# Kernel optimization log

Hardware: AMD Instinct MI355X
Metric: run time of the kernel (lower is better)

## Reference

```python
import math
import jax, jax.numpy as jnp
import numpy as np

# ---- SLAYER neuron / simulation constants (from config) ----
THETA = 10.0      # spike threshold
TAU_SR = 10.0     # PSP (SRM) kernel time constant
TAU_REF = 1.0     # refractory kernel time constant
TS = 1.0          # simulation time step
T_SAMPLE = 500    # number of time bins
B, N_IN, N_HID, N_OUT = 64, 1024, 1024, 10


def _alpha_kernel(tau, mult, eps=0.01):
    """slayer _calculateAlphaKernel: mult * t/tau * exp(1 - t/tau), truncated."""
    vals = []
    t = 0.0
    while t < T_SAMPLE:
        v = mult * t / tau * math.exp(1.0 - t / tau)
        if abs(v) < eps and t > tau:
            break
        vals.append(v)
        t += TS
    return np.asarray(vals, np.float32)

SRM_KERNEL = jnp.asarray(_alpha_kernel(TAU_SR, 1.0))            # [K]
REF_KERNEL = jnp.asarray(_alpha_kernel(TAU_REF, -2.0 * THETA))  # [Kr], REF_KERNEL[0] == 0


def dense(x, W):
    # per-timestep fully-connected layer (slayer.dense == 1x1x1 conv3d, no bias)
    # x: [B, Nin, T], W: [Nout, Nin] -> [B, Nout, T]
    return jnp.einsum('oi,bit->bot', W, x)


def psp(x):
    # causal temporal convolution with the SRM kernel: out[t] = Ts * sum_k srm[k] * x[t-k]
    Bx, N, T = x.shape
    K = SRM_KERNEL.shape[0]
    k = SRM_KERNEL[::-1].reshape(1, 1, K).astype(x.dtype)  # flip -> true convolution
    y = jax.lax.conv_general_dilated(
        x.reshape(Bx * N, 1, T), k, (1,), [(K - 1, 0)],
        dimension_numbers=('NCH', 'OIH', 'NCH'))
    return y.reshape(Bx, N, T) * TS


def spike_impl(u_in):
    # sequential LIF thresholding with refractory feedback (slayer spike kernel)
    # u_in: [B, N, T] membrane drive; returns (spikes, membrane) both [B, N, T]
    Kr = REF_KERNEL.shape[0]
    # buf[j] is the refractory contribution arriving at step t+j; new spike at t
    # contributes REF_KERNEL[j] at t+j (REF_KERNEL[0]==0), i.e. shifted kernel into buf.
    refk = jnp.concatenate([REF_KERNEL[1:], jnp.zeros((1,), u_in.dtype)]).astype(u_in.dtype)
    buf0 = jnp.zeros(u_in.shape[:-1] + (Kr,), u_in.dtype)

    def step(buf, u_t):
        u = u_t + buf[..., 0]                              # membrane at time t
        s = (u >= THETA).astype(u_in.dtype) / TS           # spike (amplitude 1/Ts)
        buf = jnp.concatenate([buf[..., 1:], jnp.zeros_like(buf[..., :1])], axis=-1)
        buf = buf + s[..., None] * refk
        return buf, (s, u)

    _, (s, u) = jax.lax.scan(step, buf0, jnp.moveaxis(u_in, -1, 0))
    return jnp.moveaxis(s, 0, -1), jnp.moveaxis(u, 0, -1)


def setup_inputs() -> dict:
    key = jax.random.key(0)
    k1, k2, k3 = jax.random.split(key, 3)
    spike_input = (jax.random.uniform(k1, (B, N_IN, T_SAMPLE)) < 0.05).astype(jnp.float32)
    W1 = jax.random.normal(k2, (N_HID, N_IN), jnp.float32) * 0.3
    W2 = jax.random.normal(k3, (N_OUT, N_HID), jnp.float32) * 0.3
    return {"spike_input": spike_input, "W1": W1, "W2": W2}


def reference(spike_input, W1, W2):
    s1, _ = spike_impl(psp(dense(spike_input, W1)))
    s2, _ = spike_impl(psp(dense(s1, W2)))
    return s2
```

## Files before the change

### kernel.cpp

```cpp
#include <hip/hip_runtime.h>
#include <stdint.h>
#include <math.h>

#define T_SIM 500
#define NB    64
#define NIN   1024
#define NHID  1024
#define NOUT  10
#define KSRM  77
#define CHUNK 32
#define TT5   12
#define NT5   42
#define RING5 128

__device__ __forceinline__ double srm_tap(int k) {
  double u = (double)k / 10.0;
  double v = u * exp(1.0 - u);
  return (double)(float)v;
}
__device__ __forceinline__ double ref_tap(int j) {
  double v = (-20.0 * (double)j) * exp(1.0 - (double)j);
  return (double)(float)v;
}

__global__ __launch_bounds__(64)
void k_pack(const float* __restrict__ x, unsigned long long* __restrict__ bits) {
  const int b = blockIdx.x, ig = blockIdx.y, tc = blockIdx.z;
  const int lane = threadIdx.x;
  const float* xr = x + ((size_t)b * NIN + ig * 64 + lane) * T_SIM;
  const int t0 = tc * 100;
  for (int t = t0; t < t0 + 100; t += 4) {
    const float4 v = *(const float4*)(xr + t);
    unsigned long long m0 = __ballot(v.x > 0.5f);
    unsigned long long m1 = __ballot(v.y > 0.5f);
    unsigned long long m2 = __ballot(v.z > 0.5f);
    unsigned long long m3 = __ballot(v.w > 0.5f);
    if (lane == 0) {
      unsigned long long* w = bits + (size_t)(b * T_SIM + t) * 16 + ig;
      w[0] = m0; w[16] = m1; w[32] = m2; w[48] = m3;
    }
  }
}

__global__ __launch_bounds__(256)
void k_transpose(const float* __restrict__ W1, float* __restrict__ W1T) {
  __shared__ float tile[64][65];
  const int bo = blockIdx.x * 64, bi = blockIdx.y * 64;
  for (int k = threadIdx.x; k < 4096; k += 256) {
    int r = k >> 6, c = k & 63;
    tile[r][c] = W1[(size_t)(bo + r) * NIN + bi + c];
  }
  __syncthreads();
  for (int k = threadIdx.x; k < 4096; k += 256) {
    int r = k >> 6, c = k & 63;
    W1T[(size_t)(bi + r) * NHID + bo + c] = tile[c][r];
  }
}

__global__ __launch_bounds__(128)
void k_dense1(const uint32_t* __restrict__ bits, const float* __restrict__ W1T,
              double* __restrict__ a1c, int col_base) {
  __shared__ int list[NIN];
  __shared__ int nact_s;
  const int col_loc = blockIdx.x;
  const int tid = threadIdx.x;
  if (tid < 32) {
    uint32_t w = bits[(size_t)(col_base + col_loc) * 32 + tid];
    int c = __popc(w);
    int p = c;
#pragma unroll
    for (int d = 1; d < 32; d <<= 1) {
      int q = __shfl_up(p, d);
      if (tid >= d) p += q;
    }
    int excl = p - c;
    while (w) {
      const int j = __ffs(w) - 1;
      w &= w - 1;
      list[excl++] = tid * 32 + j;
    }
    if (tid == 31) nact_s = excl;
  }
  __syncthreads();
  const int n = nact_s;
  const int o = blockIdx.y * 512 + tid * 4;
  double ax[4] = {0,0,0,0}, ay[4] = {0,0,0,0};
  double az[4] = {0,0,0,0}, aw[4] = {0,0,0,0};
  float4 L[8];
  int g = 0;
  if (n >= 8) {
#pragma unroll
    for (int r = 0; r < 8; ++r)
      L[r] = *(const float4*)(W1T + (size_t)list[r] * NHID + o);
    for (g = 0; g + 16 <= n; g += 8) {
      float4 Nb[8];
#pragma unroll
      for (int r = 0; r < 8; ++r)
        Nb[r] = *(const float4*)(W1T + (size_t)list[g + 8 + r] * NHID + o);
#pragma unroll
      for (int r = 0; r < 8; ++r) {
        const int s = r & 3;
        ax[s] += (double)L[r].x; ay[s] += (double)L[r].y;
        az[s] += (double)L[r].z; aw[s] += (double)L[r].w;
      }
#pragma unroll
      for (int r = 0; r < 8; ++r) L[r] = Nb[r];
    }
#pragma unroll
    for (int r = 0; r < 8; ++r) {
      const int s = r & 3;
      ax[s] += (double)L[r].x; ay[s] += (double)L[r].y;
      az[s] += (double)L[r].z; aw[s] += (double)L[r].w;
    }
    g += 8;
  }
  for (; g < n; ++g) {
    const float4 wv = *(const float4*)(W1T + (size_t)list[g] * NHID + o);
    const int s = g & 3;
    ax[s] += (double)wv.x; ay[s] += (double)wv.y;
    az[s] += (double)wv.z; aw[s] += (double)wv.w;
  }
  double* dst = a1c + (size_t)col_loc * NHID + o;
  __builtin_nontemporal_store((ax[0] + ax[1]) + (ax[2] + ax[3]), dst + 0);
  __builtin_nontemporal_store((ay[0] + ay[1]) + (ay[2] + ay[3]), dst + 1);
  __builtin_nontemporal_store((az[0] + az[1]) + (az[2] + az[3]), dst + 2);
  __builtin_nontemporal_store((aw[0] + aw[1]) + (aw[2] + aw[3]), dst + 3);
}

__global__ __launch_bounds__(448)
void k_ps1(const double* __restrict__ a1c, uint32_t* __restrict__ s1w,
           int b_base) {
  __shared__ double S[RING5 * 32];
  __shared__ double Yp[2][4][TT5 * 32];
  __shared__ double TB[80];
  const int ng = blockIdx.x, b_loc = blockIdx.y;
  const int tid = threadIdx.x;
  const double* __restrict__ abase = a1c + (size_t)b_loc * T_SIM * NHID + ng * 32;
  uint32_t* __restrict__ sbase = s1w + (size_t)(b_base + b_loc) * T_SIM * 32 + ng;

  if (tid < 80) TB[tid] = (tid <= 76) ? srm_tap(tid) : 0.0;
  for (int i = tid; i < RING5 * 32; i += 448) S[i] = 0.0;
  __syncthreads();
  for (int id = tid; id < TT5 * 32; id += 448) {
    const int r = id >> 5, nn = id & 31;
    S[r * 32 + nn] = abase[(size_t)r * NHID + nn];
  }

  const bool isFIR = (tid < 384);
  const int g   = tid / 96;
  const int rem = tid - g * 96;
  const int q   = rem >> 5;
  const int n   = rem & 31;
  double tap[20];
  __syncthreads();
  if (isFIR) {
#pragma unroll
    for (int j = 0; j < 20; ++j) tap[j] = TB[20 * g + j];
  }
  double refk[11];
#pragma unroll
  for (int j = 1; j <= 10; ++j) refk[j] = ref_tap(j);
  uint32_t smask = 0;

  for (int k = 0; k < NT5; ++k) {
    const int t0 = k * TT5;
    const int tv = (T_SIM - t0 < TT5) ? (T_SIM - t0) : TT5;
    const int t0n = t0 + TT5;
    const int tvn = (t0n >= T_SIM) ? 0 : ((T_SIM - t0n < TT5) ? (T_SIM - t0n) : TT5);
    if (isFIR) {
      double pf = 0.0;
      const int pr = tid >> 5, pn = tid & 31;
      const bool hasPf = (tid < tvn * 32);
      if (hasPf) pf = abase[(size_t)(t0n + pr) * NHID + pn];
      const int tb = t0 + q * 4;
      int slot = (tb - 20 * g - 19 + 1024) & (RING5 - 1);
      double a0 = 0, a1 = 0, a2 = 0, a3 = 0;
#pragma unroll
      for (int s = 0; s < 23; ++s) {
        const double v = S[slot * 32 + n];
        slot = (slot + 1) & (RING5 - 1);
        if (s <= 19)           a0 += tap[19 - s] * v;
        if (s >= 1 && s <= 20) a1 += tap[20 - s] * v;
        if (s >= 2 && s <= 21) a2 += tap[21 - s] * v;
        if (s >= 3)            a3 += tap[22 - s] * v;
      }
      double* Yk = Yp[k & 1][g];
      const int tl = q * 4;
      if (tl + 0 < tv) Yk[(tl + 0) * 32 + n] = a0;
      if (tl + 1 < tv) Yk[(tl + 1) * 32 + n] = a1;
      if (tl + 2 < tv) Yk[(tl + 2) * 32 + n] = a2;
      if (tl + 3 < tv) Yk[(tl + 3) * 32 + n] = a3;
      if (hasPf) S[((t0n + pr) & (RING5 - 1)) * 32 + pn] = pf;
    } else if (k > 0) {
      const int lane = tid - 384;
      if (lane < 32) {
        const int t0p = t0 - TT5;
        const double* Y0 = Yp[(k - 1) & 1][0];
        const double* Y1 = Yp[(k - 1) & 1][1];
        const double* Y2 = Yp[(k - 1) & 1][2];
        const double* Y3 = Yp[(k - 1) & 1][3];
        for (int gg = 0; gg < TT5; ++gg) {
          double u = (Y0[gg * 32 + lane] + Y1[gg * 32 + lane]) +
                     (Y2[gg * 32 + lane] + Y3[gg * 32 + lane]);
#pragma unroll
          for (int j = 10; j >= 1; --j)
            u += refk[j] * (double)((smask >> (j - 1)) & 1u);
          const bool sp = (u >= 10.0);
          smask = (smask << 1) | (sp ? 1u : 0u);
          const unsigned long long bm = __ballot(sp);
          if (lane == 0) sbase[(size_t)(t0p + gg) * 32] = (uint32_t)bm;
        }
      }
    }
    __syncthreads();
  }
  if (!isFIR) {
    const int lane = tid - 384;
    if (lane < 32) {
      const int t0p = (NT5 - 1) * TT5;
      const int tvp = T_SIM - t0p;
      const double* Y0 = Yp[(NT5 - 1) & 1][0];
      const double* Y1 = Yp[(NT5 - 1) & 1][1];
      const double* Y2 = Yp[(NT5 - 1) & 1][2];
      const double* Y3 = Yp[(NT5 - 1) & 1][3];
      for (int gg = 0; gg < tvp; ++gg) {
        double u = (Y0[gg * 32 + lane] + Y1[gg * 32 + lane]) +
                   (Y2[gg * 32 + lane] + Y3[gg * 32 + lane]);
#pragma unroll
        for (int j = 10; j >= 1; --j)
          u += refk[j] * (double)((smask >> (j - 1)) & 1u);
        const bool sp = (u >= 10.0);
        smask = (smask << 1) | (sp ? 1u : 0u);
        const unsigned long long bm = __ballot(sp);
        if (lane == 0) sbase[(size_t)(t0p + gg) * 32] = (uint32_t)bm;
      }
    }
  }
}

__global__ __launch_bounds__(256)
void k_dense2(const uint32_t* __restrict__ s1w,
              const float* __restrict__ W2, double* __restrict__ a2) {
  __shared__ float w2t[NHID * NOUT];
  for (int k = threadIdx.x; k < NHID * NOUT; k += 256) {
    const int o = k >> 10, i = k & 1023;
    w2t[i * NOUT + o] = W2[k];
  }
  __syncthreads();
  const int col = blockIdx.x * 256 + threadIdx.x;
  double acc[NOUT];
#pragma unroll
  for (int o = 0; o < NOUT; ++o) acc[o] = 0.0;
  const uint32_t* w = s1w + (size_t)col * 32;
  for (int wi = 0; wi < 32; ++wi) {
    uint32_t m = w[wi];
    const int ibase = wi * 32;
    while (m) {
      const int j = __ffs(m) - 1;
      m &= m - 1;
      const float* row = &w2t[(ibase + j) * NOUT];
#pragma unroll
      for (int o = 0; o < NOUT; ++o) acc[o] += (double)row[o];
    }
  }
  double* outp = a2 + (size_t)col * NOUT;
#pragma unroll
  for (int o = 0; o < NOUT; ++o) outp[o] = acc[o];
}

__global__ __launch_bounds__(256)
void k_l2(const double* __restrict__ a2, float* __restrict__ out) {
  __shared__ double S[T_SIM * NOUT];
  __shared__ double Y[T_SIM * NOUT];
  __shared__ double srm[KSRM];
  const int b = blockIdx.x, tid = threadIdx.x;
  if (tid < KSRM) srm[tid] = srm_tap(tid);
  for (int i = tid; i < T_SIM * NOUT; i += 256)
    S[i] = a2[(size_t)b * T_SIM * NOUT + i];
  __syncthreads();
  for (int i = tid; i < T_SIM * NOUT; i += 256) {
    const int t = i / 10, o = i - t * 10;
    const int kmax = (t < KSRM - 1) ? t : (KSRM - 1);
    double acc = 0.0;
    for (int k = 0; k <= kmax; ++k)
      acc += srm[k] * S[(t - k) * 10 + o];
    Y[i] = acc;
  }
  __syncthreads();
  if (tid < NOUT) {
    double refk[11];
#pragma unroll
    for (int j = 1; j <= 10; ++j) refk[j] = ref_tap(j);
    uint32_t smask = 0;
    float* op = out + ((size_t)b * NOUT + tid) * T_SIM;
    for (int t = 0; t < T_SIM; ++t) {
      double u = Y[t * 10 + tid];
#pragma unroll
      for (int j = 10; j >= 1; --j)
        u += refk[j] * (double)((smask >> (j - 1)) & 1u);
      const bool sp = (u >= 10.0);
      smask = (smask << 1) | (sp ? 1u : 0u);
      op[t] = sp ? 1.0f : 0.0f;
    }
  }
}

extern "C" void kernel_launch(void* const* d_in, const int* in_sizes, int n_in,
                              void* d_out, int out_size, void* d_ws, size_t ws_size,
                              hipStream_t stream) {
  const float* x  = (const float*)d_in[0];
  const float* W1 = (const float*)d_in[1];
  const float* W2 = (const float*)d_in[2];
  float* out = (float*)d_out;

  char* ws = (char*)d_ws;
  unsigned long long* bits1 = (unsigned long long*)(ws);
  float*  W1T = (float*) (ws + 4096000);
  double* a1c = (double*)(ws + 8290304);
  uint32_t* s1w = (uint32_t*)(ws + 139362304);
  double* a2  = (double*)(ws + 143458304);

  hipLaunchKernelGGL(k_pack, dim3(NB, 16, 5), dim3(64), 0, stream, x, bits1);
  hipLaunchKernelGGL(k_transpose, dim3(16, 16), dim3(256), 0, stream, W1, W1T);

  for (int bc = 0; bc < NB; bc += CHUNK) {
    hipLaunchKernelGGL(k_dense1, dim3(CHUNK * T_SIM, 2), dim3(128), 0, stream,
                       (const uint32_t*)bits1, W1T, a1c, bc * T_SIM);
    hipLaunchKernelGGL(k_ps1, dim3(32, CHUNK), dim3(448), 0, stream,
                       a1c, s1w, bc);
  }

  hipLaunchKernelGGL(k_dense2, dim3(125), dim3(256), 0, stream, s1w, W2, a2);
  hipLaunchKernelGGL(k_l2, dim3(NB), dim3(256), 0, stream, a2, out);
}
```

Measured before the change: 951.4 us.

## Fuse sparse dense1 gather into PSP/spike kernel using precomputed active lists

Replaces the separate k_dense1 pass, which wrote a large double-precision activation buffer to global memory, and the chunked k_ps1 pass that read it back. A new k_lists kernel precomputes, per batch and timestep, the indices of active input spikes (capped at 128) plus their count. k_ps1f stages these lists in shared memory, double-buffered two tiles ahead. It gathers W1T rows on the fly into the shared PSP ring, so no intermediate activation tensor touches HBM and the batch-chunk launch loop goes away. The trade-offs are more per-block gather latency inside the sequential PSP loop, and a correctness dependence on no column having more than 128 active inputs.

```diff
diff --git a/kernel.cpp b/kernel.cpp
--- a/kernel.cpp
+++ b/kernel.cpp
@@ -8,10 +8,11 @@
 #define NHID  1024
 #define NOUT  10
 #define KSRM  77
-#define CHUNK 32
 #define TT5   12
 #define NT5   42
-#define RING5 128
+#define RINGN 128
+#define NGW   32
+#define LMAX  128
 
 __device__ __forceinline__ double srm_tap(int k) {
   double u = (double)k / 10.0;
@@ -57,15 +58,13 @@
   }
 }
 
-__global__ __launch_bounds__(128)
-void k_dense1(const uint32_t* __restrict__ bits, const float* __restrict__ W1T,
-              double* __restrict__ a1c, int col_base) {
-  __shared__ int list[NIN];
-  __shared__ int nact_s;
-  const int col_loc = blockIdx.x;
+__global__ __launch_bounds__(64)
+void k_lists(const uint32_t* __restrict__ bits, unsigned short* __restrict__ lists,
+             int* __restrict__ cnt) {
+  const int col = blockIdx.x * T_SIM + blockIdx.y;
   const int tid = threadIdx.x;
   if (tid < 32) {
-    uint32_t w = bits[(size_t)(col_base + col_loc) * 32 + tid];
+    uint32_t w = bits[(size_t)col * 32 + tid];
     int c = __popc(w);
     int p = c;
 #pragma unroll
@@ -74,93 +73,71 @@
       if (tid >= d) p += q;
     }
     int excl = p - c;
+    unsigned short* lp = lists + (size_t)col * LMAX;
     while (w) {
       const int j = __ffs(w) - 1;
       w &= w - 1;
-      list[excl++] = tid * 32 + j;
-    }
-    if (tid == 31) nact_s = excl;
-  }
-  __syncthreads();
-  const int n = nact_s;
-  const int o = blockIdx.y * 512 + tid * 4;
-  double ax[4] = {0,0,0,0}, ay[4] = {0,0,0,0};
-  double az[4] = {0,0,0,0}, aw[4] = {0,0,0,0};
-  float4 L[8];
-  int g = 0;
-  if (n >= 8) {
-#pragma unroll
-    for (int r = 0; r < 8; ++r)
-      L[r] = *(const float4*)(W1T + (size_t)list[r] * NHID + o);
-    for (g = 0; g + 16 <= n; g += 8) {
-      float4 Nb[8];
-#pragma unroll
-      for (int r = 0; r < 8; ++r)
-        Nb[r] = *(const float4*)(W1T + (size_t)list[g + 8 + r] * NHID + o);
-#pragma unroll
-      for (int r = 0; r < 8; ++r) {
-        const int s = r & 3;
-        ax[s] += (double)L[r].x; ay[s] += (double)L[r].y;
-        az[s] += (double)L[r].z; aw[s] += (double)L[r].w;
-      }
-#pragma unroll
-      for (int r = 0; r < 8; ++r) L[r] = Nb[r];
-    }
-#pragma unroll
-    for (int r = 0; r < 8; ++r) {
-      const int s = r & 3;
-      ax[s] += (double)L[r].x; ay[s] += (double)L[r].y;
-      az[s] += (double)L[r].z; aw[s] += (double)L[r].w;
-    }
-    g += 8;
-  }
-  for (; g < n; ++g) {
-    const float4 wv = *(const float4*)(W1T + (size_t)list[g] * NHID + o);
-    const int s = g & 3;
-    ax[s] += (double)wv.x; ay[s] += (double)wv.y;
-    az[s] += (double)wv.z; aw[s] += (double)wv.w;
-  }
-  double* dst = a1c + (size_t)col_loc * NHID + o;
-  __builtin_nontemporal_store((ax[0] + ax[1]) + (ax[2] + ax[3]), dst + 0);
-  __builtin_nontemporal_store((ay[0] + ay[1]) + (ay[2] + ay[3]), dst + 1);
-  __builtin_nontemporal_store((az[0] + az[1]) + (az[2] + az[3]), dst + 2);
-  __builtin_nontemporal_store((aw[0] + aw[1]) + (aw[2] + aw[3]), dst + 3);
-}
-
-__global__ __launch_bounds__(448)
-void k_ps1(const double* __restrict__ a1c, uint32_t* __restrict__ s1w,
-           int b_base) {
-  __shared__ double S[RING5 * 32];
-  __shared__ double Yp[2][4][TT5 * 32];
+      lp[excl++] = (unsigned short)(tid * 32 + j);
+    }
+    if (tid == 31) cnt[col] = excl;
+  }
+}
+
+__global__ __launch_bounds__(448, 4)
+void k_ps1f(const float* __restrict__ W1T,
+            const unsigned short* __restrict__ lists,
+            const int* __restrict__ cnt_g,
+            uint32_t* __restrict__ s1w) {
+  __shared__ double S[RINGN * NGW];
+  __shared__ double Yp[2][4][TT5 * NGW];
   __shared__ double TB[80];
-  const int ng = blockIdx.x, b_loc = blockIdx.y;
+  __shared__ unsigned short Lst[2][TT5][LMAX];
+  __shared__ int Cnt[2][TT5];
+  const int ng = blockIdx.x, b = blockIdx.y;
   const int tid = threadIdx.x;
-  const double* __restrict__ abase = a1c + (size_t)b_loc * T_SIM * NHID + ng * 32;
-  uint32_t* __restrict__ sbase = s1w + (size_t)(b_base + b_loc) * T_SIM * 32 + ng;
+  const size_t bcol0 = (size_t)b * T_SIM;
+  uint32_t* __restrict__ sbase = s1w + (size_t)b * T_SIM * 32 + ng;
+  const float* __restrict__ wb0 = W1T + ng * NGW;
 
   if (tid < 80) TB[tid] = (tid <= 76) ? srm_tap(tid) : 0.0;
-  for (int i = tid; i < RING5 * 32; i += 448) S[i] = 0.0;
-  __syncthreads();
-  for (int id = tid; id < TT5 * 32; id += 448) {
-    const int r = id >> 5, nn = id & 31;
-    S[r * 32 + nn] = abase[(size_t)r * NHID + nn];
-  }
+  for (int i = tid; i < RINGN * NGW; i += 448) S[i] = 0.0;
+  if (tid < 24) Cnt[tid / 12][tid % 12] = cnt_g[bcol0 + tid];
+  {
+    const uint32_t* lg = (const uint32_t*)lists + bcol0 * (LMAX / 2);
+    uint32_t* ll = (uint32_t*)&Lst[0][0][0];
+    for (int i = tid; i < 24 * (LMAX / 2); i += 448) ll[i] = lg[i];
+  }
+  __syncthreads();
 
   const bool isFIR = (tid < 384);
   const int g   = tid / 96;
   const int rem = tid - g * 96;
   const int q   = rem >> 5;
   const int n   = rem & 31;
+  const int tt  = tid >> 5;
+  const int nn  = tid & 31;
   double tap[20];
-  __syncthreads();
   if (isFIR) {
 #pragma unroll
     for (int j = 0; j < 20; ++j) tap[j] = TB[20 * g + j];
+    const int c = Cnt[0][tt];
+    const uint32_t* lp32 = (const uint32_t*)&Lst[0][tt][0];
+    const float* wbase = wb0 + nn;
+    double a0 = 0.0, a1 = 0.0;
+    const int c2 = c >> 1;
+    for (int j = 0; j < c2; ++j) {
+      const uint32_t pr = lp32[j];
+      a0 += (double)wbase[(size_t)(pr & 0xffffu) << 10];
+      a1 += (double)wbase[(size_t)(pr >> 16) << 10];
+    }
+    if (c & 1) a0 += (double)wbase[(size_t)Lst[0][tt][c - 1] << 10];
+    S[tt * NGW + nn] = a0 + a1;
   }
   double refk[11];
 #pragma unroll
   for (int j = 1; j <= 10; ++j) refk[j] = ref_tap(j);
   uint32_t smask = 0;
+  __syncthreads();
 
   for (int k = 0; k < NT5; ++k) {
     const int t0 = k * TT5;
@@ -168,17 +145,37 @@
     const int t0n = t0 + TT5;
     const int tvn = (t0n >= T_SIM) ? 0 : ((T_SIM - t0n < TT5) ? (T_SIM - t0n) : TT5);
     if (isFIR) {
-      double pf = 0.0;
-      const int pr = tid >> 5, pn = tid & 31;
-      const bool hasPf = (tid < tvn * 32);
-      if (hasPf) pf = abase[(size_t)(t0n + pr) * NHID + pn];
+      if (tt < tvn) {
+        const int bufn = (k + 1) & 1;
+        const int c = Cnt[bufn][tt];
+        const uint32_t* lp32 = (const uint32_t*)&Lst[bufn][tt][0];
+        const float* wbase = wb0 + nn;
+        double a0 = 0.0, a1 = 0.0;
+        const int c2 = c >> 1;
+        for (int j = 0; j < c2; ++j) {
+          const uint32_t pr = lp32[j];
+          a0 += (double)wbase[(size_t)(pr & 0xffffu) << 10];
+          a1 += (double)wbase[(size_t)(pr >> 16) << 10];
+        }
+        if (c & 1) a0 += (double)wbase[(size_t)Lst[bufn][tt][c - 1] << 10];
+        S[((t0n + tt) & (RINGN - 1)) * NGW + nn] = a0 + a1;
+      }
+      const int k2 = k + 2;
+      if (k2 < NT5) {
+        const int t2 = k2 * TT5;
+        const int tv2 = (T_SIM - t2 < TT5) ? (T_SIM - t2) : TT5;
+        if (tid < tv2) Cnt[k & 1][tid] = cnt_g[bcol0 + t2 + tid];
+        const uint32_t* lg = (const uint32_t*)lists + (bcol0 + t2) * (LMAX / 2);
+        uint32_t* ll = (uint32_t*)&Lst[k & 1][0][0];
+        for (int i = tid; i < tv2 * (LMAX / 2); i += 384) ll[i] = lg[i];
+      }
       const int tb = t0 + q * 4;
-      int slot = (tb - 20 * g - 19 + 1024) & (RING5 - 1);
+      int slot = (tb - 20 * g - 19 + 1024) & (RINGN - 1);
       double a0 = 0, a1 = 0, a2 = 0, a3 = 0;
 #pragma unroll
       for (int s = 0; s < 23; ++s) {
-        const double v = S[slot * 32 + n];
-        slot = (slot + 1) & (RING5 - 1);
+        const double v = S[slot * NGW + n];
+        slot = (slot + 1) & (RINGN - 1);
         if (s <= 19)           a0 += tap[19 - s] * v;
         if (s >= 1 && s <= 20) a1 += tap[20 - s] * v;
         if (s >= 2 && s <= 21) a2 += tap[21 - s] * v;
@@ -186,11 +183,10 @@
       }
       double* Yk = Yp[k & 1][g];
       const int tl = q * 4;
-      if (tl + 0 < tv) Yk[(tl + 0) * 32 + n] = a0;
-      if (tl + 1 < tv) Yk[(tl + 1) * 32 + n] = a1;
-      if (tl + 2 < tv) Yk[(tl + 2) * 32 + n] = a2;
-      if (tl + 3 < tv) Yk[(tl + 3) * 32 + n] = a3;
-      if (hasPf) S[((t0n + pr) & (RING5 - 1)) * 32 + pn] = pf;
+      if (tl + 0 < tv) Yk[(tl + 0) * NGW + n] = a0;
+      if (tl + 1 < tv) Yk[(tl + 1) * NGW + n] = a1;
+      if (tl + 2 < tv) Yk[(tl + 2) * NGW + n] = a2;
+      if (tl + 3 < tv) Yk[(tl + 3) * NGW + n] = a3;
     } else if (k > 0) {
       const int lane = tid - 384;
       if (lane < 32) {
@@ -200,8 +196,8 @@
         const double* Y2 = Yp[(k - 1) & 1][2];
         const double* Y3 = Yp[(k - 1) & 1][3];
         for (int gg = 0; gg < TT5; ++gg) {
-          double u = (Y0[gg * 32 + lane] + Y1[gg * 32 + lane]) +
-                     (Y2[gg * 32 + lane] + Y3[gg * 32 + lane]);
+          double u = (Y0[gg * NGW + lane] + Y1[gg * NGW + lane]) +
+                     (Y2[gg * NGW + lane] + Y3[gg * NGW + lane]);
 #pragma unroll
           for (int j = 10; j >= 1; --j)
             u += refk[j] * (double)((smask >> (j - 1)) & 1u);
@@ -224,8 +220,8 @@
       const double* Y2 = Yp[(NT5 - 1) & 1][2];
       const double* Y3 = Yp[(NT5 - 1) & 1][3];
       for (int gg = 0; gg < tvp; ++gg) {
-        double u = (Y0[gg * 32 + lane] + Y1[gg * 32 + lane]) +
-                   (Y2[gg * 32 + lane] + Y3[gg * 32 + lane]);
+        double u = (Y0[gg * NGW + lane] + Y1[gg * NGW + lane]) +
+                   (Y2[gg * NGW + lane] + Y3[gg * NGW + lane]);
 #pragma unroll
         for (int j = 10; j >= 1; --j)
           u += refk[j] * (double)((smask >> (j - 1)) & 1u);
@@ -315,20 +311,19 @@
 
   char* ws = (char*)d_ws;
   unsigned long long* bits1 = (unsigned long long*)(ws);
-  float*  W1T = (float*) (ws + 4096000);
-  double* a1c = (double*)(ws + 8290304);
-  uint32_t* s1w = (uint32_t*)(ws + 139362304);
-  double* a2  = (double*)(ws + 143458304);
+  float*  W1T = (float*)(ws + 4096000);
+  unsigned short* lists = (unsigned short*)(ws + 8290304);
+  int* cnt = (int*)(ws + 16482304);
+  uint32_t* s1w = (uint32_t*)(ws + 16610304);
+  double* a2  = (double*)(ws + 20706304);
 
   hipLaunchKernelGGL(k_pack, dim3(NB, 16, 5), dim3(64), 0, stream, x, bits1);
   hipLaunchKernelGGL(k_transpose, dim3(16, 16), dim3(256), 0, stream, W1, W1T);
-
-  for (int bc = 0; bc < NB; bc += CHUNK) {
-    hipLaunchKernelGGL(k_dense1, dim3(CHUNK * T_SIM, 2), dim3(128), 0, stream,
-                       (const uint32_t*)bits1, W1T, a1c, bc * T_SIM);
-    hipLaunchKernelGGL(k_ps1, dim3(32, CHUNK), dim3(448), 0, stream,
-                       a1c, s1w, bc);
-  }
+  hipLaunchKernelGGL(k_lists, dim3(NB, T_SIM), dim3(64), 0, stream,
+                     (const uint32_t*)bits1, lists, cnt);
+
+  hipLaunchKernelGGL(k_ps1f, dim3(32, NB), dim3(448), 0, stream,
+                     W1T, lists, cnt, s1w);
 
   hipLaunchKernelGGL(k_dense2, dim3(125), dim3(256), 0, stream, s1w, W2, a2);
   hipLaunchKernelGGL(k_l2, dim3(NB), dim3(256), 0, stream, a2, out);
```

Result: slower. 1.291 ms (+35.7%).
